# Performance work log

Hardware: AMD Instinct MI355X
Metric: run time of the kernel (lower is better)

The kernel has to match this reference:

```python
import jax, jax.numpy as jnp
import numpy as np

BS, SEQ, DIN, HID, H = 2, 2048, 1024, 1024, 16
D = HID // H  # head_size = 64

def setup_inputs() -> dict:
    key = jax.random.key(0)
    ks = jax.random.split(key, 9)
    s = 0.02
    return {
        "x":    jax.random.normal(ks[0], (BS, SEQ, DIN), jnp.float32),
        "Wq":   jax.random.normal(ks[1], (DIN, HID), jnp.float32) * s,
        "bq":   jax.random.normal(ks[2], (HID,), jnp.float32) * s,
        "Wk":   jax.random.normal(ks[3], (DIN, HID), jnp.float32) * s,
        "bk":   jax.random.normal(ks[4], (HID,), jnp.float32) * s,
        "Wv":   jax.random.normal(ks[5], (DIN, HID), jnp.float32) * s,
        "bv":   jax.random.normal(ks[6], (HID,), jnp.float32) * s,
        "Wmix": jax.random.normal(ks[7], (HID, HID), jnp.float32) * s,
        "bmix": jax.random.normal(ks[8], (HID,), jnp.float32) * s,
    }

def reference(x, Wq, bq, Wk, bk, Wv, bv, Wmix, bmix):
    bs, seq, _ = x.shape
    scale = jnp.asarray(D ** 0.5, x.dtype)
    # projections, split heads: [b, s, H, D] (contiguous channel slices per head,
    # equivalent to the torch transpose/reshape dance)
    q = (x @ Wq + bq).reshape(bs, seq, H, D)
    k = (x @ Wk + bk).reshape(bs, seq, H, D)
    v = (x @ Wv + bv).reshape(bs, seq, H, D)
    scores = jnp.einsum('bqhd,bkhd->bhqk', q, k) / scale  # [b, H, seq, seq]
    causal_mask = jnp.triu(jnp.ones((seq, seq), bool), k=1)
    scores = jnp.where(causal_mask, -jnp.inf, scores)
    probs = jax.nn.softmax(scores, axis=-1)
    att = jnp.einsum('bhqk,bkhd->bqhd', probs, v).reshape(bs, seq, HID)
    return att @ Wmix + bmix
```

## Files before the change

### kernel.cpp

```cpp
#include <hip/hip_runtime.h>
#include <hip/hip_bf16.h>

#define BS 2
#define SEQ 2048
#define DIN 1024
#define HID 1024
#define NH 16
#define HD 64
#define M_ROWS (BS*SEQ)
#define NQKV 3072

typedef __attribute__((ext_vector_type(8))) short short8;
typedef __attribute__((ext_vector_type(4))) short short4v;
typedef __attribute__((ext_vector_type(8))) __bf16 bf16x8;
typedef __attribute__((ext_vector_type(4))) float floatx4;

__device__ __forceinline__ short f2bf(float f) {
  return __builtin_bit_cast(short, (__bf16)f);
}
__device__ __forceinline__ float bf2f(short s) {
  return __uint_as_float(((unsigned)(unsigned short)s) << 16);
}

__device__ __forceinline__ floatx4 mfma16(short8 a, short8 b, floatx4 c) {
  return __builtin_amdgcn_mfma_f32_16x16x32_bf16(
      __builtin_bit_cast(bf16x8, a), __builtin_bit_cast(bf16x8, b), c, 0, 0, 0);
}

__device__ __forceinline__ float exp2fast(float x) {
#if __has_builtin(__builtin_amdgcn_exp2f)
  return __builtin_amdgcn_exp2f(x);
#else
  return exp2f(x);
#endif
}

__device__ __forceinline__ void gload_lds16(const void* g, void* l) {
  __builtin_amdgcn_global_load_lds(
      (const __attribute__((address_space(1))) unsigned int*)g,
      (__attribute__((address_space(3))) unsigned int*)l, 16, 0, 0);
}

__device__ __forceinline__ int swz_off(int row, int colsh) {
  return row * 128 + ((colsh * 2) ^ ((row & 7) << 4));
}

__global__ __launch_bounds__(256) void prep_kernel(
    const float* __restrict__ x,
    const float* __restrict__ Wq, const float* __restrict__ Wk,
    const float* __restrict__ Wv, const float* __restrict__ Wmix,
    short* __restrict__ xb, short* __restrict__ Wt, short* __restrict__ Wmixt)
{
  __shared__ float Ws[64][65];
  if (blockIdx.z < 4) {
    const float* src; short* dst;
    switch (blockIdx.z) {
      case 0:  src = Wq;   dst = Wt;                 break;
      case 1:  src = Wk;   dst = Wt + (1u << 20);    break;
      case 2:  src = Wv;   dst = Wt + (2u << 20);    break;
      default: src = Wmix; dst = Wmixt;              break;
    }
    const int n0 = blockIdx.x * 64, k0 = blockIdx.y * 64;
    const int c = threadIdx.x & 63, r0 = threadIdx.x >> 6;
    #pragma unroll
    for (int i = 0; i < 16; ++i) {
      int rr = r0 + 4 * i;
      Ws[rr][c] = src[(size_t)(k0 + rr) * DIN + n0 + c];
    }
    __syncthreads();
    #pragma unroll
    for (int i = 0; i < 16; ++i) {
      int cc = r0 + 4 * i;
      dst[(size_t)(n0 + cc) * DIN + k0 + c] = f2bf(Ws[c][cc]);
    }
  } else {
    const int bb = blockIdx.y * 16 + blockIdx.x;
    const int gid0 = bb * 256 + threadIdx.x;
    const float4* x4 = (const float4*)x;
    #pragma unroll
    for (int it = 0; it < 8; ++it) {
      int gid = gid0 + it * 65536;
      float4 v0 = x4[2 * gid], v1 = x4[2 * gid + 1];
      short8 o;
      o[0] = f2bf(v0.x); o[1] = f2bf(v0.y); o[2] = f2bf(v0.z); o[3] = f2bf(v0.w);
      o[4] = f2bf(v1.x); o[5] = f2bf(v1.y); o[6] = f2bf(v1.z); o[7] = f2bf(v1.w);
      *(short8*)&xb[(size_t)gid * 8] = o;
    }
  }
}

template<int BM, int BN, bool OUT_F32, bool QKV>
__global__ __launch_bounds__(256) void gemm_kernel(
    const short* __restrict__ A, const short* __restrict__ Bt,
    const float* __restrict__ bias0, const float* __restrict__ bias1,
    const float* __restrict__ bias2, void* __restrict__ Cp,
    short* __restrict__ vt, int Ndim, int Kdim)
{
  constexpr int MT = BM / 32, NT = BN / 32;
  __shared__ short As[BM * 64];
  __shared__ short Bs[BN * 64];
  const int tid = threadIdx.x;
  const int wid = tid >> 6, lane = tid & 63, lg = lane >> 4, lm = lane & 15;
  const int wr = wid >> 1, wc = wid & 1;

  const int nwgx = gridDim.x;
  const int nwg = nwgx * gridDim.y;
  const int idlin = blockIdx.y * nwgx + blockIdx.x;
  const int sw = (idlin & 7) * (nwg >> 3) + (idlin >> 3);
  const int m0 = (sw / nwgx) * BM, n0 = (sw % nwgx) * BN;

  floatx4 acc[MT][NT];
  #pragma unroll
  for (int i = 0; i < MT; ++i)
    #pragma unroll
    for (int j = 0; j < NT; ++j) acc[i][j] = floatx4{0.f, 0.f, 0.f, 0.f};

  for (int k0 = 0; k0 < Kdim; k0 += 64) {
    __syncthreads();
    #pragma unroll
    for (int j = 0; j < BM / 32; ++j) {
      int flat = tid + 256 * j;
      int row = flat >> 3, ch = (flat & 7) ^ (row & 7);
      gload_lds16(A + (size_t)(m0 + row) * Kdim + k0 + ch * 8,
                  (char*)As + wid * 1024 + j * 4096);
    }
    #pragma unroll
    for (int j = 0; j < BN / 32; ++j) {
      int flat = tid + 256 * j;
      int row = flat >> 3, ch = (flat & 7) ^ (row & 7);
      gload_lds16(Bt + (size_t)(n0 + row) * Kdim + k0 + ch * 8,
                  (char*)Bs + wid * 1024 + j * 4096);
    }
    __syncthreads();

    #pragma unroll
    for (int kk = 0; kk < 2; ++kk) {
      short8 a[MT], b[NT];
      #pragma unroll
      for (int mt = 0; mt < MT; ++mt) {
        int row = wr * (BM / 2) + mt * 16 + lm;
        int ch = (kk * 4 + lg) ^ (row & 7);
        a[mt] = *(const short8*)&As[row * 64 + ch * 8];
      }
      #pragma unroll
      for (int nt = 0; nt < NT; ++nt) {
        int row = wc * (BN / 2) + nt * 16 + lm;
        int ch = (kk * 4 + lg) ^ (row & 7);
        b[nt] = *(const short8*)&Bs[row * 64 + ch * 8];
      }
      #pragma unroll
      for (int mt = 0; mt < MT; ++mt)
        #pragma unroll
        for (int nt = 0; nt < NT; ++nt)
          acc[mt][nt] = mfma16(a[mt], b[nt], acc[mt][nt]);
    }
  }

  #pragma unroll
  for (int mt = 0; mt < MT; ++mt) {
    const int row0 = m0 + wr * (BM / 2) + mt * 16 + 4 * lg;
    #pragma unroll
    for (int nt = 0; nt < NT; ++nt) {
      const int col = n0 + wc * (BN / 2) + nt * 16 + lm;
      const float* bp = bias0;
      if (QKV) bp = (col < 1024) ? bias0 : (col < 2048 ? bias1 : bias2);
      const float bv = bp[col & 1023];
      if (QKV && n0 >= 2048) {
        int hd = col - 2048;
        int bb = row0 >> 11, s = row0 & 2047;
        short4v pv;
        #pragma unroll
        for (int r = 0; r < 4; ++r) pv[r] = f2bf(acc[mt][nt][r] + bv);
        *(short4v*)&vt[((size_t)(bb * (NH * HD) + hd)) * SEQ + s] = pv;
      } else {
        #pragma unroll
        for (int r = 0; r < 4; ++r) {
          float v = acc[mt][nt][r] + bv;
          if (OUT_F32) ((float*)Cp)[(size_t)(row0 + r) * Ndim + col] = v;
          else         ((short*)Cp)[(size_t)(row0 + r) * Ndim + col] = f2bf(v);
        }
      }
    }
  }
}

#define MFIX 12.0f
__global__ __launch_bounds__(256, 4) void attn_kernel(
    const short* __restrict__ qkv, const short* __restrict__ vt,
    short* __restrict__ att, short* __restrict__ pO, float* __restrict__ pml)
{
  __shared__ short Ks[2 * 64 * 64];
  __shared__ short Vs[2 * 64 * 64];
  __shared__ short Ps[4 * 16 * 64];
  const int tid = threadIdx.x;
  const int wid = tid >> 6, lane = tid & 63, lg = lane >> 4, lm = lane & 15;

  int id = blockIdx.x, x, c;
  if (id < 8)       { x = id;                      c = 0;       }
  else if (id < 24) { int t = id - 8;  x = 8  + (t >> 1); c = t & 1; }
  else if (id < 48) { int t = id - 24; x = 16 + t / 3;    c = t % 3; }
  else              { int t = id - 48; x = 24 + (t >> 2); c = t & 3; }
  const int nch = (x >> 3) + 1;
  const int tb = c * 8;
  const int te = min(tb + 8, x + 1);
  const int q0 = x * 64;
  const int bh = blockIdx.y, b = bh >> 4, h = bh & 15;
  const short* qp = qkv + (size_t)(b * SEQ) * NQKV + h * HD;
  const short* kp = qp + HID;
  const short* vp = vt + (size_t)bh * HD * SEQ;

  const float cl2 = 0.18033688011112042f;
  const int qrow_g = q0 + wid * 16 + lm;
  short8 qf[2];
  {
    const short* qrow = qp + (size_t)qrow_g * NQKV;
    #pragma unroll
    for (int kk = 0; kk < 2; ++kk) {
      short8 raw = *(const short8*)(qrow + kk * 32 + lg * 8);
      #pragma unroll
      for (int j = 0; j < 8; ++j) qf[kk][j] = f2bf(bf2f(raw[j]) * cl2);
    }
  }

  short8 ones;
  #pragma unroll
  for (int j = 0; j < 8; ++j) ones[j] = (short)0x3F80;

  const int rstage = tid >> 3, c8 = (tid & 7) * 8;
  int soff[2], koff[2][4], pw[4], pr[2];
  #pragma unroll
  for (int i = 0; i < 2; ++i) soff[i] = swz_off(rstage + 32 * i, c8);
  #pragma unroll
  for (int kk = 0; kk < 2; ++kk)
    #pragma unroll
    for (int nt = 0; nt < 4; ++nt)
      koff[kk][nt] = swz_off(nt * 16 + lm, kk * 32 + lg * 8);
  #pragma unroll
  for (int nt = 0; nt < 4; ++nt) pw[nt] = swz_off(lm, nt * 16 + 4 * lg);
  #pragma unroll
  for (int kk = 0; kk < 2; ++kk) pr[kk] = swz_off(lm, kk * 32 + lg * 8);

  const short* kgp[2];
  const short* vgp[2];
  short8 kreg[2], vreg[2];
  #pragma unroll
  for (int i = 0; i < 2; ++i) {
    kgp[i] = kp + (size_t)(tb * 64 + rstage + 32 * i) * NQKV + c8;
    vgp[i] = vp + (size_t)(rstage + 32 * i) * SEQ + tb * 64 + c8;
    kreg[i] = *(const short8*)kgp[i];
    vreg[i] = *(const short8*)vgp[i];
  }

  char* psw = (char*)(Ps + wid * 16 * 64);
  floatx4 o[4];
  floatx4 ol = floatx4{0.f, 0.f, 0.f, 0.f};
  #pragma unroll
  for (int nt = 0; nt < 4; ++nt) o[nt] = floatx4{0.f, 0.f, 0.f, 0.f};

  for (int t = tb; t < te; ++t) {
    const int cb = (t - tb) & 1;
    char* Kb = (char*)Ks + cb * 8192;
    char* Vb = (char*)Vs + cb * 8192;
    #pragma unroll
    for (int i = 0; i < 2; ++i) {
      *(short8*)(Kb + soff[i]) = kreg[i];
      *(short8*)(Vb + soff[i]) = vreg[i];
    }
    if (t + 1 < te) {
      #pragma unroll
      for (int i = 0; i < 2; ++i) {
        kgp[i] += 64 * NQKV;
        vgp[i] += 64;
        kreg[i] = *(const short8*)kgp[i];
        vreg[i] = *(const short8*)vgp[i];
      }
    }
    __syncthreads();

    floatx4 s[4];
    #pragma unroll
    for (int nt = 0; nt < 4; ++nt) s[nt] = floatx4{-MFIX, -MFIX, -MFIX, -MFIX};
    __builtin_amdgcn_s_setprio(1);
    #pragma unroll
    for (int kk = 0; kk < 2; ++kk)
      #pragma unroll
      for (int nt = 0; nt < 4; ++nt)
        s[nt] = mfma16(*(const short8*)(Kb + koff[kk][nt]), qf[kk], s[nt]);
    __builtin_amdgcn_s_setprio(0);

    if (t == x) {
      #pragma unroll
      for (int nt = 0; nt < 4; ++nt)
        #pragma unroll
        for (int r = 0; r < 4; ++r) {
          int kv = t * 64 + nt * 16 + 4 * lg + r;
          if (kv > qrow_g) s[nt][r] = -3e38f;
        }
    }

    #pragma unroll
    for (int nt = 0; nt < 4; ++nt) {
      short4v pv;
      #pragma unroll
      for (int r = 0; r < 4; ++r) pv[r] = f2bf(exp2fast(s[nt][r]));
      *(short4v*)(psw + pw[nt]) = pv;
    }

    #pragma unroll
    for (int kk = 0; kk < 2; ++kk) {
      short8 pf = *(const short8*)(psw + pr[kk]);
      __builtin_amdgcn_s_setprio(1);
      #pragma unroll
      for (int nt = 0; nt < 4; ++nt)
        o[nt] = mfma16(*(const short8*)(Vb + koff[kk][nt]), pf, o[nt]);
      ol = mfma16(ones, pf, ol);
      __builtin_amdgcn_s_setprio(0);
    }
  }

  if (nch == 1) {
    const float linv = 1.0f / ol[0];
    #pragma unroll
    for (int nt = 0; nt < 4; ++nt) {
      short4v ov;
      #pragma unroll
      for (int r = 0; r < 4; ++r) ov[r] = f2bf(o[nt][r] * linv);
      *(short4v*)&att[((size_t)(b * SEQ + qrow_g)) * HID + h * HD + nt * 16 + 4 * lg] = ov;
    }
  } else {
    int off;
    if (x < 16)      off = (x - 8) * 2;
    else if (x < 24) off = 16 + (x - 16) * 3;
    else             off = 40 + (x - 24) * 4;
    const int slot = bh * 72 + off + c;
    short* po = pO + (size_t)slot * 4096;
    const int ql = wid * 16 + lm;
    #pragma unroll
    for (int nt = 0; nt < 4; ++nt) {
      short4v ov;
      #pragma unroll
      for (int r = 0; r < 4; ++r) ov[r] = f2bf(o[nt][r]);
      *(short4v*)&po[ql * 64 + nt * 16 + 4 * lg] = ov;
    }
    if (lane < 16) {
      pml[slot * 128 + 64 + ql] = ol[0];
    }
  }
}

__global__ __launch_bounds__(256) void combine_kernel(
    const short* __restrict__ pO, const float* __restrict__ pml,
    short* __restrict__ att)
{
  const int x = 8 + blockIdx.x;
  const int bh = blockIdx.y, b = bh >> 4, h = bh & 15;
  const int nch = (x >> 3) + 1;
  const int tid = threadIdx.x;
  const int row = tid >> 2, d0 = (tid & 3) * 16;
  int off;
  if (x < 16)      off = (x - 8) * 2;
  else if (x < 24) off = 16 + (x - 16) * 3;
  else             off = 40 + (x - 24) * 4;
  const int base_slot = bh * 72 + off;

  float L = 0.f;
  for (int cc = 0; cc < nch; ++cc)
    L += pml[(base_slot + cc) * 128 + 64 + row];
  const float inv = 1.0f / L;

  float acc[16];
  #pragma unroll
  for (int j = 0; j < 16; ++j) acc[j] = 0.f;
  for (int cc = 0; cc < nch; ++cc) {
    const short* po = pO + (size_t)(base_slot + cc) * 4096 + row * 64 + d0;
    short8 v0 = *(const short8*)po, v1 = *(const short8*)(po + 8);
    #pragma unroll
    for (int j = 0; j < 8; ++j) {
      acc[j]     += bf2f(v0[j]);
      acc[j + 8] += bf2f(v1[j]);
    }
  }
  short8 o0, o1;
  #pragma unroll
  for (int j = 0; j < 8; ++j) {
    o0[j] = f2bf(acc[j] * inv);
    o1[j] = f2bf(acc[j + 8] * inv);
  }
  short* dst = att + ((size_t)(b * SEQ + x * 64 + row)) * HID + h * HD + d0;
  *(short8*)dst = o0;
  *(short8*)(dst + 8) = o1;
}

extern "C" void kernel_launch(void* const* d_in, const int* in_sizes, int n_in,
                              void* d_out, int out_size, void* d_ws, size_t ws_size,
                              hipStream_t stream) {
  (void)in_sizes; (void)n_in; (void)out_size; (void)ws_size;
  const float* x    = (const float*)d_in[0];
  const float* Wq   = (const float*)d_in[1];
  const float* bq   = (const float*)d_in[2];
  const float* Wk   = (const float*)d_in[3];
  const float* bk   = (const float*)d_in[4];
  const float* Wv   = (const float*)d_in[5];
  const float* bv   = (const float*)d_in[6];
  const float* Wmix = (const float*)d_in[7];
  const float* bmix = (const float*)d_in[8];
  float* out = (float*)d_out;

  char* w = (char*)d_ws;
  short* xb      = (short*)w; w += (size_t)8 << 20;
  short* Wt      = (short*)w; w += (size_t)6 << 20;
  short* Wmixt   = (short*)w; w += (size_t)2 << 20;
  short* qkvb    = (short*)w; w += (size_t)24 << 20;
  short* vtb     = (short*)w; w += (size_t)8 << 20;
  short* ab      = (short*)w; w += (size_t)8 << 20;
  short* pO      = (short*)w; w += (size_t)72 * 32 * 4096 * 2;
  float* pml     = (float*)w;

  hipLaunchKernelGGL(prep_kernel, dim3(16, 16, 5), dim3(256), 0, stream,
                     x, Wq, Wk, Wv, Wmix, xb, Wt, Wmixt);

  hipLaunchKernelGGL((gemm_kernel<128, 128, false, true>), dim3(NQKV / 128, M_ROWS / 128),
                     dim3(256), 0, stream, xb, Wt, bq, bk, bv, (void*)qkvb, vtb, NQKV, DIN);

  hipLaunchKernelGGL(attn_kernel, dim3(80, BS * NH), dim3(256), 0, stream,
                     qkvb, vtb, ab, pO, pml);
  hipLaunchKernelGGL(combine_kernel, dim3(24, BS * NH), dim3(256), 0, stream,
                     pO, pml, ab);

  hipLaunchKernelGGL((gemm_kernel<64, 128, true, false>), dim3(HID / 128, M_ROWS / 64),
                     dim3(256), 0, stream, ab, Wmixt, bmix, bmix, bmix, (void*)out,
                     (short*)nullptr, HID, DIN);
}
```

Measured before the change: 100.2 us.

## Split attention KV tile across wave pairs with 32-row query tiles and LDS reduction

Reorganises the attention block so each wave handles 32 query rows and half of the 64-key tile, loading K/V fragments once into registers and reusing them across two query subtiles. Partial outputs from the two key halves are reduced through LDS at the end. K/V double buffering is dropped in favour of a single buffer with an extra barrier per iteration. The aim is to cut redundant LDS reads of K/V per MFMA. The trade-offs are more registers, an added synchronisation per tile, and an extra reduction step at the end.

After: 103.2 us (median of 2 runs). +3.0%, slower.

```diff
diff --git a/kernel.cpp b/kernel.cpp
--- a/kernel.cpp
+++ b/kernel.cpp
@@ -43,6 +43,9 @@
 
 __device__ __forceinline__ int swz_off(int row, int colsh) {
   return row * 128 + ((colsh * 2) ^ ((row & 7) << 4));
+}
+__device__ __forceinline__ int swz256(int row, int bytecol) {
+  return row * 256 + (bytecol ^ ((row & 7) << 4));
 }
 
 __global__ __launch_bounds__(256) void prep_kernel(
@@ -189,11 +192,13 @@
     const short* __restrict__ qkv, const short* __restrict__ vt,
     short* __restrict__ att, short* __restrict__ pO, float* __restrict__ pml)
 {
-  __shared__ short Ks[2 * 64 * 64];
-  __shared__ short Vs[2 * 64 * 64];
-  __shared__ short Ps[4 * 16 * 64];
+  __shared__ short Ks[64 * 64];
+  __shared__ short Vs[64 * 64];
+  __shared__ short Ps[4 * 32 * 64];
+  __shared__ float Lb[2][32];
   const int tid = threadIdx.x;
   const int wid = tid >> 6, lane = tid & 63, lg = lane >> 4, lm = lane & 15;
+  const int kh = wid & 1, qh = wid >> 1;
 
   int id = blockIdx.x, x, c;
   if (id < 8)       { x = id;                      c = 0;       }
@@ -210,15 +215,17 @@
   const short* vp = vt + (size_t)bh * HD * SEQ;
 
   const float cl2 = 0.18033688011112042f;
-  const int qrow_g = q0 + wid * 16 + lm;
-  short8 qf[2];
-  {
-    const short* qrow = qp + (size_t)qrow_g * NQKV;
+  int qg[2];
+  short8 qf[2][2];
+  #pragma unroll
+  for (int qt = 0; qt < 2; ++qt) {
+    qg[qt] = q0 + qh * 32 + qt * 16 + lm;
+    const short* qrow = qp + (size_t)qg[qt] * NQKV;
     #pragma unroll
     for (int kk = 0; kk < 2; ++kk) {
       short8 raw = *(const short8*)(qrow + kk * 32 + lg * 8);
       #pragma unroll
-      for (int j = 0; j < 8; ++j) qf[kk][j] = f2bf(bf2f(raw[j]) * cl2);
+      for (int j = 0; j < 8; ++j) qf[qt][kk][j] = f2bf(bf2f(raw[j]) * cl2);
     }
   }
 
@@ -227,18 +234,24 @@
   for (int j = 0; j < 8; ++j) ones[j] = (short)0x3F80;
 
   const int rstage = tid >> 3, c8 = (tid & 7) * 8;
-  int soff[2], koff[2][4], pw[4], pr[2];
+  int soff[2], koff[2][2], voff[4], pw[2][2], pr[2];
   #pragma unroll
   for (int i = 0; i < 2; ++i) soff[i] = swz_off(rstage + 32 * i, c8);
   #pragma unroll
-  for (int kk = 0; kk < 2; ++kk)
-    #pragma unroll
-    for (int nt = 0; nt < 4; ++nt)
-      koff[kk][nt] = swz_off(nt * 16 + lm, kk * 32 + lg * 8);
-  #pragma unroll
-  for (int nt = 0; nt < 4; ++nt) pw[nt] = swz_off(lm, nt * 16 + 4 * lg);
-  #pragma unroll
-  for (int kk = 0; kk < 2; ++kk) pr[kk] = swz_off(lm, kk * 32 + lg * 8);
+  for (int kvt = 0; kvt < 2; ++kvt)
+    #pragma unroll
+    for (int kk = 0; kk < 2; ++kk)
+      koff[kvt][kk] = swz_off(kh * 32 + kvt * 16 + lm, kk * 32 + lg * 8);
+  #pragma unroll
+  for (int nt = 0; nt < 4; ++nt)
+    voff[nt] = swz_off(nt * 16 + lm, kh * 32 + lg * 8);
+  #pragma unroll
+  for (int kvt = 0; kvt < 2; ++kvt)
+    #pragma unroll
+    for (int qt = 0; qt < 2; ++qt)
+      pw[kvt][qt] = swz_off(qt * 16 + lm, kvt * 16 + 4 * lg);
+  #pragma unroll
+  for (int qt = 0; qt < 2; ++qt) pr[qt] = swz_off(qt * 16 + lm, lg * 8);
 
   const short* kgp[2];
   const short* vgp[2];
@@ -251,20 +264,20 @@
     vreg[i] = *(const short8*)vgp[i];
   }
 
-  char* psw = (char*)(Ps + wid * 16 * 64);
-  floatx4 o[4];
-  floatx4 ol = floatx4{0.f, 0.f, 0.f, 0.f};
-  #pragma unroll
-  for (int nt = 0; nt < 4; ++nt) o[nt] = floatx4{0.f, 0.f, 0.f, 0.f};
+  char* psw = (char*)(Ps + wid * 32 * 64);
+  floatx4 o[4][2];
+  floatx4 ol[2] = {floatx4{0.f, 0.f, 0.f, 0.f}, floatx4{0.f, 0.f, 0.f, 0.f}};
+  #pragma unroll
+  for (int nt = 0; nt < 4; ++nt)
+    #pragma unroll
+    for (int qt = 0; qt < 2; ++qt) o[nt][qt] = floatx4{0.f, 0.f, 0.f, 0.f};
 
   for (int t = tb; t < te; ++t) {
-    const int cb = (t - tb) & 1;
-    char* Kb = (char*)Ks + cb * 8192;
-    char* Vb = (char*)Vs + cb * 8192;
+    __syncthreads();
     #pragma unroll
     for (int i = 0; i < 2; ++i) {
-      *(short8*)(Kb + soff[i]) = kreg[i];
-      *(short8*)(Vb + soff[i]) = vreg[i];
+      *(short8*)((char*)Ks + soff[i]) = kreg[i];
+      *(short8*)((char*)Vs + soff[i]) = vreg[i];
     }
     if (t + 1 < te) {
       #pragma unroll
@@ -277,55 +290,106 @@
     }
     __syncthreads();
 
-    floatx4 s[4];
-    #pragma unroll
-    for (int nt = 0; nt < 4; ++nt) s[nt] = floatx4{-MFIX, -MFIX, -MFIX, -MFIX};
+    short8 kf[2][2];
+    #pragma unroll
+    for (int kvt = 0; kvt < 2; ++kvt)
+      #pragma unroll
+      for (int kk = 0; kk < 2; ++kk)
+        kf[kvt][kk] = *(const short8*)((char*)Ks + koff[kvt][kk]);
+    floatx4 s[2][2];
+    #pragma unroll
+    for (int kvt = 0; kvt < 2; ++kvt)
+      #pragma unroll
+      for (int qt = 0; qt < 2; ++qt) s[kvt][qt] = floatx4{-MFIX, -MFIX, -MFIX, -MFIX};
     __builtin_amdgcn_s_setprio(1);
     #pragma unroll
     for (int kk = 0; kk < 2; ++kk)
       #pragma unroll
+      for (int kvt = 0; kvt < 2; ++kvt)
+        #pragma unroll
+        for (int qt = 0; qt < 2; ++qt)
+          s[kvt][qt] = mfma16(kf[kvt][kk], qf[qt][kk], s[kvt][qt]);
+    __builtin_amdgcn_s_setprio(0);
+
+    if (t == x) {
+      #pragma unroll
+      for (int kvt = 0; kvt < 2; ++kvt)
+        #pragma unroll
+        for (int qt = 0; qt < 2; ++qt)
+          #pragma unroll
+          for (int r = 0; r < 4; ++r) {
+            int kv = t * 64 + kh * 32 + kvt * 16 + 4 * lg + r;
+            if (kv > qg[qt]) s[kvt][qt][r] = -3e38f;
+          }
+    }
+
+    #pragma unroll
+    for (int kvt = 0; kvt < 2; ++kvt)
+      #pragma unroll
+      for (int qt = 0; qt < 2; ++qt) {
+        short4v pv;
+        #pragma unroll
+        for (int r = 0; r < 4; ++r) pv[r] = f2bf(exp2fast(s[kvt][qt][r]));
+        *(short4v*)(psw + pw[kvt][qt]) = pv;
+      }
+
+    short8 vf[4];
+    #pragma unroll
+    for (int nt = 0; nt < 4; ++nt)
+      vf[nt] = *(const short8*)((char*)Vs + voff[nt]);
+    #pragma unroll
+    for (int qt = 0; qt < 2; ++qt) {
+      short8 pf = *(const short8*)(psw + pr[qt]);
+      __builtin_amdgcn_s_setprio(1);
+      #pragma unroll
       for (int nt = 0; nt < 4; ++nt)
-        s[nt] = mfma16(*(const short8*)(Kb + koff[kk][nt]), qf[kk], s[nt]);
-    __builtin_amdgcn_s_setprio(0);
-
-    if (t == x) {
-      #pragma unroll
-      for (int nt = 0; nt < 4; ++nt)
-        #pragma unroll
-        for (int r = 0; r < 4; ++r) {
-          int kv = t * 64 + nt * 16 + 4 * lg + r;
-          if (kv > qrow_g) s[nt][r] = -3e38f;
-        }
-    }
-
+        o[nt][qt] = mfma16(vf[nt], pf, o[nt][qt]);
+      ol[qt] = mfma16(ones, pf, ol[qt]);
+      __builtin_amdgcn_s_setprio(0);
+    }
+  }
+
+  __syncthreads();
+  float* Ob = (float*)Ps;
+  if (kh == 1) {
+    #pragma unroll
+    for (int qt = 0; qt < 2; ++qt) {
+      #pragma unroll
+      for (int nt = 0; nt < 4; ++nt) {
+        int row = qh * 32 + qt * 16 + lm;
+        *(floatx4*)((char*)Ob + swz256(row, (nt * 16 + 4 * lg) * 4)) = o[nt][qt];
+      }
+      if (lg == 0) Lb[qh][qt * 16 + lm] = ol[qt][0];
+    }
+  }
+  __syncthreads();
+  if (kh == 1) return;
+
+  float lpart[2];
+  #pragma unroll
+  for (int qt = 0; qt < 2; ++qt) {
     #pragma unroll
     for (int nt = 0; nt < 4; ++nt) {
-      short4v pv;
-      #pragma unroll
-      for (int r = 0; r < 4; ++r) pv[r] = f2bf(exp2fast(s[nt][r]));
-      *(short4v*)(psw + pw[nt]) = pv;
-    }
-
-    #pragma unroll
-    for (int kk = 0; kk < 2; ++kk) {
-      short8 pf = *(const short8*)(psw + pr[kk]);
-      __builtin_amdgcn_s_setprio(1);
-      #pragma unroll
-      for (int nt = 0; nt < 4; ++nt)
-        o[nt] = mfma16(*(const short8*)(Vb + koff[kk][nt]), pf, o[nt]);
-      ol = mfma16(ones, pf, ol);
-      __builtin_amdgcn_s_setprio(0);
-    }
+      int row = qh * 32 + qt * 16 + lm;
+      floatx4 v = *(const floatx4*)((const char*)Ob + swz256(row, (nt * 16 + 4 * lg) * 4));
+      #pragma unroll
+      for (int r = 0; r < 4; ++r) o[nt][qt][r] += v[r];
+    }
+    lpart[qt] = ol[qt][0] + Lb[qh][qt * 16 + lm];
   }
 
   if (nch == 1) {
-    const float linv = 1.0f / ol[0];
-    #pragma unroll
-    for (int nt = 0; nt < 4; ++nt) {
-      short4v ov;
-      #pragma unroll
-      for (int r = 0; r < 4; ++r) ov[r] = f2bf(o[nt][r] * linv);
-      *(short4v*)&att[((size_t)(b * SEQ + qrow_g)) * HID + h * HD + nt * 16 + 4 * lg] = ov;
+    #pragma unroll
+    for (int qt = 0; qt < 2; ++qt) {
+      const float linv = 1.0f / lpart[qt];
+      short* dst = att + ((size_t)(b * SEQ + qg[qt])) * HID + h * HD;
+      #pragma unroll
+      for (int nt = 0; nt < 4; ++nt) {
+        short4v ov;
+        #pragma unroll
+        for (int r = 0; r < 4; ++r) ov[r] = f2bf(o[nt][qt][r] * linv);
+        *(short4v*)(dst + nt * 16 + 4 * lg) = ov;
+      }
     }
   } else {
     int off;
@@ -334,16 +398,17 @@
     else             off = 40 + (x - 24) * 4;
     const int slot = bh * 72 + off + c;
     short* po = pO + (size_t)slot * 4096;
-    const int ql = wid * 16 + lm;
-    #pragma unroll
-    for (int nt = 0; nt < 4; ++nt) {
-      short4v ov;
-      #pragma unroll
-      for (int r = 0; r < 4; ++r) ov[r] = f2bf(o[nt][r]);
-      *(short4v*)&po[ql * 64 + nt * 16 + 4 * lg] = ov;
-    }
-    if (lane < 16) {
-      pml[slot * 128 + 64 + ql] = ol[0];
+    #pragma unroll
+    for (int qt = 0; qt < 2; ++qt) {
+      const int ql = qh * 32 + qt * 16 + lm;
+      #pragma unroll
+      for (int nt = 0; nt < 4; ++nt) {
+        short4v ov;
+        #pragma unroll
+        for (int r = 0; r < 4; ++r) ov[r] = f2bf(o[nt][qt][r]);
+        *(short4v*)&po[ql * 64 + nt * 16 + 4 * lg] = ov;
+      }
+      if (lg == 0) pml[slot * 128 + 64 + ql] = lpart[qt];
     }
   }
 }
```
